# Kernel optimization log

Hardware: AMD Instinct MI355X
Metric: run time of the kernel (lower is better)

Reference implementation:

```python
import jax, jax.numpy as jnp
import numpy as np

NUM_USERS = 100000
NUM_ITEMS = 100000
D = 64
B, P, N, NB, NN = 1024, 32, 64, 32, 32
W1, W2, W3 = 1.0, 0.1, 1.0


def setup_inputs() -> dict:
    key = jax.random.key(0)
    ks = jax.random.split(key, 12)
    u2e = 0.1 + 0.03 * jax.random.normal(ks[0], (NUM_USERS, D), jnp.float32)
    v2e = 0.1 + 0.03 * jax.random.normal(ks[1], (NUM_ITEMS, D), jnp.float32)
    margin_uv = jnp.ones((NUM_USERS, 1), jnp.float32)
    margin_vv = jnp.ones((NUM_ITEMS, 1), jnp.float32)
    margin_uu = jnp.ones((NUM_USERS, 1), jnp.float32)
    train_u = jax.random.randint(ks[2], (B,), 0, NUM_USERS)
    pos_idx = jax.random.randint(ks[3], (B, P), 0, NUM_ITEMS)
    neg_idx = jax.random.randint(ks[4], (B, N), 0, NUM_ITEMS)
    nb_idx = jax.random.randint(ks[5], (B, NB), 0, NUM_USERS)
    nn_idx = jax.random.randint(ks[6], (B, NN), 0, NUM_USERS)
    # ragged lengths -> padded masks
    def mk_mask(k, maxlen):
        lens = jax.random.randint(k, (B,), 1, maxlen + 1)
        return jnp.arange(maxlen)[None, :] < lens[:, None]
    pos_mask = mk_mask(ks[7], P)
    neg_mask = mk_mask(ks[8], N)
    nb_mask = mk_mask(ks[9], NB)
    nn_mask = mk_mask(ks[10], NN)
    return dict(u2e=u2e, v2e=v2e, margin_uv=margin_uv, margin_vv=margin_vv,
                margin_uu=margin_uu, train_u=train_u, pos_idx=pos_idx,
                neg_idx=neg_idx, nb_idx=nb_idx, nn_idx=nn_idx,
                pos_mask=pos_mask, neg_mask=neg_mask, nb_mask=nb_mask,
                nn_mask=nn_mask)


def reference(u2e, v2e, margin_uv, margin_vv, margin_uu, train_u, pos_idx,
              neg_idx, nb_idx, nn_idx, pos_mask, neg_mask, nb_mask, nn_mask):
    u_e = u2e[train_u]            # [B,D]
    p_e = v2e[pos_idx]            # [B,P,D]
    n_e = v2e[neg_idx]            # [B,N,D]
    nb_e = u2e[nb_idx]            # [B,NB,D]
    nn_e = u2e[nn_idx]            # [B,NN,D]
    pm = pos_mask.astype(u_e.dtype)
    nm = neg_mask.astype(u_e.dtype)
    nbm = nb_mask.astype(u_e.dtype)
    nnm = nn_mask.astype(u_e.dtype)

    # user-item triplet loss: hinge[b,i,k] = m_u[b] + ||u-p_i||^2 - ||u-n_k||^2
    d1 = jnp.sum((u_e[:, None, :] - p_e) ** 2, -1)   # [B,P]
    d2 = jnp.sum((u_e[:, None, :] - n_e) ** 2, -1)   # [B,N]
    m_u = margin_uv[train_u, 0]                       # [B]
    uv = jax.nn.relu(m_u[:, None, None] + d1[:, :, None] - d2[:, None, :])
    uv_loss = jnp.sum(uv * (pm[:, :, None] * nm[:, None, :]))

    # item-item loss (torch broadcast: margin over a separate positive axis j)
    # hinge[b,i,j,k] = m_v[b,j] + ||p_i-u||^2 - ||p_i-n_k||^2
    p2 = jnp.sum(p_e ** 2, -1)                        # [B,P]
    n2 = jnp.sum(n_e ** 2, -1)                        # [B,N]
    d2v = p2[:, :, None] + n2[:, None, :] - 2.0 * jnp.einsum('bpd,bnd->bpn', p_e, n_e)
    m_v = margin_vv[pos_idx, 0]                       # [B,P]
    hinge_vv = jax.nn.relu(m_v[:, None, :, None] + d1[:, :, None, None] - d2v[:, :, None, :])
    mask_vv = pm[:, :, None, None] * pm[:, None, :, None] * nm[:, None, None, :]
    vv_loss = jnp.sum(hinge_vv * mask_vv)

    # user-user social loss
    d1s = jnp.sum((u_e[:, None, :] - nb_e) ** 2, -1)  # [B,NB]
    d2s = jnp.sum((u_e[:, None, :] - nn_e) ** 2, -1)  # [B,NN]
    m_s = margin_uu[train_u, 0]                       # [B]
    uu = jax.nn.relu(m_s[:, None, None] + d1s[:, :, None] - d2s[:, None, :])
    uu_loss = jnp.sum(uu * (nbm[:, :, None] * nnm[:, None, :]))

    # margin regularizer (masked mean over batch positives)
    loss_am = (jnp.mean(margin_uv[train_u])
               + jnp.sum(m_v * pm) / jnp.sum(pm)
               + jnp.mean(margin_uu[train_u]))

    return uv_loss + W1 * vv_loss + W3 * uu_loss + W2 * loss_am
```

## Files before the change

kernel.cpp:

```cpp
#include <hip/hip_runtime.h>
#include <cfloat>

#define BB   1024
#define PP   32
#define NNEG 64
#define DD   64
#define BSTR 72
#define SSTR 66

static constexpr float W2c = 0.1f;

typedef __attribute__((ext_vector_type(8)))  short bf16x8;
typedef __attribute__((ext_vector_type(16))) float f32x16;

__device__ __forceinline__ short f2bf(float f) {
    unsigned u = __float_as_uint(f);
    unsigned r = (u + 0x7fffu + ((u >> 16) & 1u)) >> 16;
    return (short)r;
}

__device__ __forceinline__ float parse_mask(const void* p, int flag, int j) {
    if (flag == 1) return ((const unsigned char*)p)[j] ? 1.0f : 0.0f;
    if (flag == 2) return (((const float*)p)[j] != 0.0f) ? 1.0f : 0.0f;
    return ((const int*)p)[j] ? 1.0f : 0.0f;
}

__global__ __launch_bounds__(512, 8) void loss_kernel(
    const float* __restrict__ u2e, const float* __restrict__ v2e,
    const float* __restrict__ margin_uv, const float* __restrict__ margin_vv,
    const float* __restrict__ margin_uu,
    const int* __restrict__ train_u, const int* __restrict__ pos_idx,
    const int* __restrict__ neg_idx, const int* __restrict__ nb_idx,
    const int* __restrict__ nn_idx,
    const void* __restrict__ pos_mask, const void* __restrict__ neg_mask,
    const void* __restrict__ nb_mask, const void* __restrict__ nn_mask,
    float* __restrict__ ws) {

    const int b = blockIdx.x;
    const int t = threadIdx.x;
    const int lane = t & 63;
    const int w = t >> 6;

    __shared__ __align__(16) short pn_bf[96 * BSTR];
    __shared__ __align__(16) float s_lds[PP * SSTR];
    __shared__ float d1[PP], p2s[PP], d2[NNEG], n2s[NNEG], d1sA[PP], d2sA[PP];
    __shared__ float pmf[PP], nmf[NNEG], nbmf[PP], nnmf[PP];
    __shared__ float mvp[PP], mv_arr[PP], s_srt[PP], S_suf[PP + 1];
    __shared__ float sc[2];
    __shared__ float red[8][3];

    int flag = 0;
    if (w < 3) {
        unsigned f32h = 0, byth = 0;
        #pragma unroll
        for (int i2 = 0; i2 < 16; ++i2) {
            unsigned mw = ((const unsigned int*)pos_mask)[lane + 64 * i2];
            f32h |= (mw == 0x3f800000u) ? 1u : 0u;
            byth |= ((mw != 0x3f800000u) && (mw & 0xFFFFFF00u)) ? 1u : 0u;
        }
        flag = __any(f32h) ? 2 : (__any(byth) ? 1 : 0);
    }

    const int tu  = train_u[b];
    const int q   = t & 15;
    const int R0  = t >> 4;
    const int gi0 = pos_idx[b * PP + R0];
    const int gi1 = neg_idx[b * NNEG + R0];
    const int gi2 = neg_idx[b * NNEG + R0 + 32];
    const int row = t >> 3, sub = t & 7;
    const int sidx = (row < PP) ? nb_idx[b * PP + row] : nn_idx[b * PP + row - PP];

    const float* uR = u2e + (size_t)tu * DD;
    const float4 u4 = *(const float4*)(uR + 4 * q);
    float4 ch0 = *(const float4*)(v2e + (size_t)gi0 * DD + 4 * q);
    float4 ch1 = *(const float4*)(v2e + (size_t)gi1 * DD + 4 * q);
    float4 ch2 = *(const float4*)(v2e + (size_t)gi2 * DD + 4 * q);
    const float* rp = u2e + (size_t)sidx * DD + 8 * sub;
    const float4 e0 = *(const float4*)(rp);
    const float4 e1 = *(const float4*)(rp + 4);
    const float4 v0 = *(const float4*)(uR + 8 * sub);
    const float4 v1 = *(const float4*)(uR + 8 * sub + 4);

    {
        float sdp[3], sqp[3];
        float dx, dy, dz, dw;
        dx = ch0.x-u4.x; dy = ch0.y-u4.y; dz = ch0.z-u4.z; dw = ch0.w-u4.w;
        sdp[0] = dx*dx+dy*dy+dz*dz+dw*dw;
        sqp[0] = ch0.x*ch0.x+ch0.y*ch0.y+ch0.z*ch0.z+ch0.w*ch0.w;
        dx = ch1.x-u4.x; dy = ch1.y-u4.y; dz = ch1.z-u4.z; dw = ch1.w-u4.w;
        sdp[1] = dx*dx+dy*dy+dz*dz+dw*dw;
        sqp[1] = ch1.x*ch1.x+ch1.y*ch1.y+ch1.z*ch1.z+ch1.w*ch1.w;
        dx = ch2.x-u4.x; dy = ch2.y-u4.y; dz = ch2.z-u4.z; dw = ch2.w-u4.w;
        sdp[2] = dx*dx+dy*dy+dz*dz+dw*dw;
        sqp[2] = ch2.x*ch2.x+ch2.y*ch2.y+ch2.z*ch2.z+ch2.w*ch2.w;
        #pragma unroll
        for (int m = 1; m < 16; m <<= 1) {
            #pragma unroll
            for (int r = 0; r < 3; ++r) {
                sdp[r] += __shfl_xor(sdp[r], m);
                sqp[r] += __shfl_xor(sqp[r], m);
            }
        }
        if (q == 0) {
            d1[R0]      = sdp[0]; p2s[R0]      = sqp[0];
            d2[R0]      = sdp[1]; n2s[R0]      = sqp[1];
            d2[R0 + 32] = sdp[2]; n2s[R0 + 32] = sqp[2];
        }
    }
    {
        float dx = e0.x-v0.x, dy = e0.y-v0.y, dz = e0.z-v0.z, dw = e0.w-v0.w;
        float s = dx*dx+dy*dy+dz*dz+dw*dw;
        dx = e1.x-v1.x; dy = e1.y-v1.y; dz = e1.z-v1.z; dw = e1.w-v1.w;
        s += dx*dx+dy*dy+dz*dz+dw*dw;
        s += __shfl_xor(s, 1);
        s += __shfl_xor(s, 2);
        s += __shfl_xor(s, 4);
        if (sub == 0) { if (row < PP) d1sA[row] = s; else d2sA[row - PP] = s; }
    }
    if (t < PP) {
        float pm = parse_mask(pos_mask, flag, b * PP + t);
        float mv = margin_vv[pos_idx[b * PP + t]];
        pmf[t] = pm; mv_arr[t] = mv;
        mvp[t] = (pm != 0.0f) ? mv : -FLT_MAX;
    } else if (t < 96) {
        nmf[t - PP] = parse_mask(neg_mask, flag, b * NNEG + (t - PP));
    } else if (t < 128) {
        nbmf[t - 96] = parse_mask(nb_mask, flag, b * PP + (t - 96));
    } else if (t < 160) {
        nnmf[t - 128] = parse_mask(nn_mask, flag, b * PP + (t - 128));
    }
    if (t == 0) { sc[0] = margin_uv[tu]; sc[1] = margin_uu[tu]; }
    {
        short4 s0 = make_short4(f2bf(ch0.x), f2bf(ch0.y), f2bf(ch0.z), f2bf(ch0.w));
        short4 s1 = make_short4(f2bf(ch1.x), f2bf(ch1.y), f2bf(ch1.z), f2bf(ch1.w));
        short4 s2 = make_short4(f2bf(ch2.x), f2bf(ch2.y), f2bf(ch2.z), f2bf(ch2.w));
        *(short4*)(pn_bf + R0 * BSTR + 4 * q)        = s0;
        *(short4*)(pn_bf + (R0 + 32) * BSTR + 4 * q) = s1;
        *(short4*)(pn_bf + (R0 + 64) * BSTR + 4 * q) = s2;
    }
    __syncthreads();

    if (w < 2) {
        f32x16 acc;
        #pragma unroll
        for (int i = 0; i < 16; ++i) acc[i] = 0.0f;
        const int lr = lane & 31;
        const int hi = lane >> 5;
        const short* ap = pn_bf + lr * BSTR;
        const short* bp = pn_bf + (PP + 32 * w + lr) * BSTR;
        #pragma unroll
        for (int c = 0; c < 4; ++c) {
            const int d0 = 16 * c + 8 * hi;
            bf16x8 a   = *(const bf16x8*)(ap + d0);
            bf16x8 bfr = *(const bf16x8*)(bp + d0);
            acc = __builtin_amdgcn_mfma_f32_32x32x16_bf16(a, bfr, acc, 0, 0, 0);
        }
        #pragma unroll
        for (int r = 0; r < 16; ++r) {
            const int m = (r & 3) + 8 * (r >> 2) + 4 * hi;
            s_lds[m * SSTR + 32 * w + lr] = acc[r];
        }
    } else if (w == 2 && lane < PP) {
        float vj = mvp[lane];
        int r = 0;
        #pragma unroll
        for (int j = 0; j < PP; ++j) {
            float o = mvp[j];
            r += (o < vj || (o == vj && j < lane)) ? 1 : 0;
        }
        s_srt[r] = vj;
        __threadfence_block();
        float y = s_srt[lane];
        #pragma unroll
        for (int d = 1; d < PP; d <<= 1) {
            float z = __shfl_down(y, d);
            if (lane + d < PP) y += z;
        }
        S_suf[lane] = y;
        if (lane == 0) S_suf[PP] = 0.0f;
    }
    __syncthreads();

    const float m_u = sc[0], m_s = sc[1];
    const float s31 = s_srt[PP - 1];
    const int kb = t & 15;
    const int i  = R0;
    const float d1i = d1[i], p2i = p2s[i], pmi = pmf[i];
    float loss = 0.0f;
    #pragma unroll
    for (int c = 0; c < 4; ++c) {
        const int k = kb + 16 * c;
        const float Sik = s_lds[i * SSTR + k];
        const float cc = d1i - (p2i + n2s[k] - 2.0f * Sik);
        const float v = -cc;
        int t0 = 0;
        #pragma unroll
        for (int st = 16; st > 0; st >>= 1)
            t0 += (s_srt[t0 + st - 1] <= v) ? st : 0;
        t0 += (s31 <= v) ? 1 : 0;
        const float inner = S_suf[t0] + (float)(PP - t0) * cc;
        const float uvh = fmaxf(m_u + d1i - d2[k], 0.0f);
        loss += pmi * nmf[k] * (inner + uvh);
    }

    #pragma unroll
    for (int rr = 0; rr < 2; ++rr) {
        int pid = t + 512 * rr;
        int ii = pid >> 5, k = pid & 31;
        loss += nbmf[ii] * nnmf[k] * fmaxf(m_s + d1sA[ii] - d2sA[k], 0.0f);
    }

    float a2 = (t < PP) ? mv_arr[t] * pmf[t] : 0.0f;
    float a3 = (t < PP) ? pmf[t] : 0.0f;
    #pragma unroll
    for (int m = 1; m < 64; m <<= 1) {
        loss += __shfl_xor(loss, m);
        a2   += __shfl_xor(a2, m);
        a3   += __shfl_xor(a3, m);
    }
    if (lane == 0) { red[w][0] = loss; red[w][1] = a2; red[w][2] = a3; }
    __syncthreads();
    if (t == 0) {
        float S0 = 0, S2 = 0, S3 = 0;
        #pragma unroll
        for (int i2 = 0; i2 < 8; ++i2) { S0 += red[i2][0]; S2 += red[i2][1]; S3 += red[i2][2]; }
        ws[0 * BB + b] = S0;
        ws[1 * BB + b] = sc[0];
        ws[2 * BB + b] = S2;
        ws[3 * BB + b] = S3;
        ws[4 * BB + b] = sc[1];
    }
}

__global__ __launch_bounds__(64) void finalize_kernel(const float* __restrict__ ws,
                                                      float* __restrict__ out) {
    const int lane = threadIdx.x;
    float s[5];
    #pragma unroll
    for (int a = 0; a < 5; ++a) {
        const float4* w4 = (const float4*)(ws + a * BB);
        float acc = 0.0f;
        #pragma unroll
        for (int j = 0; j < 4; ++j) {
            float4 v = w4[lane + 64 * j];
            acc += v.x + v.y + v.z + v.w;
        }
        s[a] = acc;
    }
    #pragma unroll
    for (int m = 1; m < 64; m <<= 1)
        #pragma unroll
        for (int a = 0; a < 5; ++a) s[a] += __shfl_xor(s[a], m);
    if (lane == 0) {
        float loss_am = s[1] / (float)BB + s[2] / s[3] + s[4] / (float)BB;
        out[0] = s[0] + W2c * loss_am;
    }
}

extern "C" void kernel_launch(void* const* d_in, const int* in_sizes, int n_in,
                              void* d_out, int out_size, void* d_ws, size_t ws_size,
                              hipStream_t stream) {
    const float* u2e       = (const float*)d_in[0];
    const float* v2e       = (const float*)d_in[1];
    const float* margin_uv = (const float*)d_in[2];
    const float* margin_vv = (const float*)d_in[3];
    const float* margin_uu = (const float*)d_in[4];
    const int*   train_u   = (const int*)d_in[5];
    const int*   pos_idx   = (const int*)d_in[6];
    const int*   neg_idx   = (const int*)d_in[7];
    const int*   nb_idx    = (const int*)d_in[8];
    const int*   nn_idx    = (const int*)d_in[9];
    const void*  pos_mask  = d_in[10];
    const void*  neg_mask  = d_in[11];
    const void*  nb_mask   = d_in[12];
    const void*  nn_mask   = d_in[13];

    float* ws  = (float*)d_ws;
    float* out = (float*)d_out;

    loss_kernel<<<BB, 512, 0, stream>>>(u2e, v2e, margin_uv, margin_vv, margin_uu,
                                        train_u, pos_idx, neg_idx, nb_idx, nn_idx,
                                        pos_mask, neg_mask, nb_mask, nn_mask, ws);
    finalize_kernel<<<1, 64, 0, stream>>>(ws, out);
}
```

Baseline: 19.84 us.

## Consume MFMA accumulators in registers and drop the final block barrier

The loss kernel now evaluates the hinge/rank-search loss directly on the MFMA accumulator registers instead of spilling the P×N dot products to LDS. This removes the s_lds buffer, one __syncthreads, and the block-wide reduction. Work is split by wave: waves 0-1 handle item losses, waves 2-3 the social loss, and wave 4 the margin sums, with each wave writing partials straight to the workspace. The margin sort and suffix-scan move into wave 0 ahead of the MFMA barrier, the mask-type probe reads fewer words, and finalize uses 256 threads to reduce the larger partial array. The cost is idle waves 5-7 and a heavier serial tail on waves 0-1.

Result: slower. 21.04 us (+6.0%).

```diff
diff --git a/kernel.cpp b/kernel.cpp
--- a/kernel.cpp
+++ b/kernel.cpp
@@ -6,7 +6,11 @@
 #define NNEG 64
 #define DD   64
 #define BSTR 72
-#define SSTR 66
+
+#define WS_MU 4096
+#define WS_A2 5120
+#define WS_A3 6144
+#define WS_MS 7168
 
 static constexpr float W2c = 0.1f;
 
@@ -42,18 +46,15 @@
     const int w = t >> 6;
 
     __shared__ __align__(16) short pn_bf[96 * BSTR];
-    __shared__ __align__(16) float s_lds[PP * SSTR];
     __shared__ float d1[PP], p2s[PP], d2[NNEG], n2s[NNEG], d1sA[PP], d2sA[PP];
     __shared__ float pmf[PP], nmf[NNEG], nbmf[PP], nnmf[PP];
     __shared__ float mvp[PP], mv_arr[PP], s_srt[PP], S_suf[PP + 1];
-    __shared__ float sc[2];
-    __shared__ float red[8][3];
 
     int flag = 0;
     if (w < 3) {
         unsigned f32h = 0, byth = 0;
         #pragma unroll
-        for (int i2 = 0; i2 < 16; ++i2) {
+        for (int i2 = 0; i2 < 4; ++i2) {
             unsigned mw = ((const unsigned int*)pos_mask)[lane + 64 * i2];
             f32h |= (mw == 0x3f800000u) ? 1u : 0u;
             byth |= ((mw != 0x3f800000u) && (mw & 0xFFFFFF00u)) ? 1u : 0u;
@@ -117,19 +118,45 @@
         s += __shfl_xor(s, 4);
         if (sub == 0) { if (row < PP) d1sA[row] = s; else d2sA[row - PP] = s; }
     }
-    if (t < PP) {
-        float pm = parse_mask(pos_mask, flag, b * PP + t);
-        float mv = margin_vv[pos_idx[b * PP + t]];
-        pmf[t] = pm; mv_arr[t] = mv;
-        mvp[t] = (pm != 0.0f) ? mv : -FLT_MAX;
-    } else if (t < 96) {
-        nmf[t - PP] = parse_mask(neg_mask, flag, b * NNEG + (t - PP));
-    } else if (t < 128) {
-        nbmf[t - 96] = parse_mask(nb_mask, flag, b * PP + (t - 96));
-    } else if (t < 160) {
-        nnmf[t - 128] = parse_mask(nn_mask, flag, b * PP + (t - 128));
-    }
-    if (t == 0) { sc[0] = margin_uv[tu]; sc[1] = margin_uu[tu]; }
+    if (w == 0) {
+        if (lane < PP) {
+            float pm = parse_mask(pos_mask, flag, b * PP + lane);
+            float mv = margin_vv[pos_idx[b * PP + lane]];
+            pmf[lane] = pm; mv_arr[lane] = mv;
+            mvp[lane] = (pm != 0.0f) ? mv : -FLT_MAX;
+        } else {
+            nmf[lane - PP] = parse_mask(neg_mask, flag, b * NNEG + (lane - PP));
+        }
+    } else if (w == 1) {
+        if (lane < PP) nmf[PP + lane] = parse_mask(neg_mask, flag, b * NNEG + PP + lane);
+        else           nbmf[lane - PP] = parse_mask(nb_mask, flag, b * PP + (lane - PP));
+    } else if (w == 2 && lane < PP) {
+        nnmf[lane] = parse_mask(nn_mask, flag, b * PP + lane);
+    }
+    if (w == 0) {
+        __threadfence_block();
+        if (lane < PP) {
+            float vj = mvp[lane];
+            int r = 0;
+            #pragma unroll
+            for (int j = 0; j < PP; ++j) {
+                float o = mvp[j];
+                r += (o < vj || (o == vj && j < lane)) ? 1 : 0;
+            }
+            s_srt[r] = vj;
+        }
+        __threadfence_block();
+        if (lane < PP) {
+            float y = s_srt[lane];
+            #pragma unroll
+            for (int d = 1; d < PP; d <<= 1) {
+                float z = __shfl_down(y, d);
+                if (lane + d < PP) y += z;
+            }
+            S_suf[lane] = y;
+            if (lane == 0) S_suf[PP] = 0.0f;
+        }
+    }
     {
         short4 s0 = make_short4(f2bf(ch0.x), f2bf(ch0.y), f2bf(ch0.z), f2bf(ch0.w));
         short4 s1 = make_short4(f2bf(ch1.x), f2bf(ch1.y), f2bf(ch1.z), f2bf(ch1.w));
@@ -155,105 +182,92 @@
             bf16x8 bfr = *(const bf16x8*)(bp + d0);
             acc = __builtin_amdgcn_mfma_f32_32x32x16_bf16(a, bfr, acc, 0, 0, 0);
         }
+        const float m_u = margin_uv[tu];
+        const int   k   = 32 * w + lr;
+        const float d2k = d2[k], n2k = n2s[k], nmk = nmf[k];
+        const float s31 = s_srt[PP - 1];
+        float loss = 0.0f;
         #pragma unroll
         for (int r = 0; r < 16; ++r) {
-            const int m = (r & 3) + 8 * (r >> 2) + 4 * hi;
-            s_lds[m * SSTR + 32 * w + lr] = acc[r];
-        }
-    } else if (w == 2 && lane < PP) {
-        float vj = mvp[lane];
-        int r = 0;
-        #pragma unroll
-        for (int j = 0; j < PP; ++j) {
-            float o = mvp[j];
-            r += (o < vj || (o == vj && j < lane)) ? 1 : 0;
-        }
-        s_srt[r] = vj;
-        __threadfence_block();
-        float y = s_srt[lane];
-        #pragma unroll
-        for (int d = 1; d < PP; d <<= 1) {
-            float z = __shfl_down(y, d);
-            if (lane + d < PP) y += z;
-        }
-        S_suf[lane] = y;
-        if (lane == 0) S_suf[PP] = 0.0f;
-    }
-    __syncthreads();
-
-    const float m_u = sc[0], m_s = sc[1];
-    const float s31 = s_srt[PP - 1];
-    const int kb = t & 15;
-    const int i  = R0;
-    const float d1i = d1[i], p2i = p2s[i], pmi = pmf[i];
-    float loss = 0.0f;
+            const int i = (r & 3) + 8 * (r >> 2) + 4 * hi;
+            const float cc = d1[i] - (p2s[i] + n2k - 2.0f * acc[r]);
+            const float v = -cc;
+            int t0 = 0;
+            #pragma unroll
+            for (int st = 16; st > 0; st >>= 1)
+                t0 += (s_srt[t0 + st - 1] <= v) ? st : 0;
+            t0 += (s31 <= v) ? 1 : 0;
+            const float inner = S_suf[t0] + (float)(PP - t0) * cc;
+            const float uvh = fmaxf(m_u + d1[i] - d2k, 0.0f);
+            loss += pmf[i] * nmk * (inner + uvh);
+        }
+        #pragma unroll
+        for (int m = 1; m < 64; m <<= 1) loss += __shfl_xor(loss, m);
+        if (lane == 0) ws[b * 4 + w] = loss;
+        if (w == 0 && lane == 0) {
+            ws[WS_MU + b] = m_u;
+            ws[WS_MS + b] = margin_uu[tu];
+        }
+    } else if (w < 4) {
+        const float m_s = margin_uu[tu];
+        const int base = (w - 2) * 512;
+        float loss = 0.0f;
+        #pragma unroll
+        for (int j2 = 0; j2 < 8; ++j2) {
+            const int pid = base + lane + 64 * j2;
+            const int ii = pid >> 5, k = pid & 31;
+            loss += nbmf[ii] * nnmf[k] * fmaxf(m_s + d1sA[ii] - d2sA[k], 0.0f);
+        }
+        #pragma unroll
+        for (int m = 1; m < 64; m <<= 1) loss += __shfl_xor(loss, m);
+        if (lane == 0) ws[b * 4 + w] = loss;
+    } else if (w == 4) {
+        float a2 = (lane < PP) ? mv_arr[lane] * pmf[lane] : 0.0f;
+        float a3 = (lane < PP) ? pmf[lane] : 0.0f;
+        #pragma unroll
+        for (int m = 1; m < 64; m <<= 1) {
+            a2 += __shfl_xor(a2, m);
+            a3 += __shfl_xor(a3, m);
+        }
+        if (lane == 0) { ws[WS_A2 + b] = a2; ws[WS_A3 + b] = a3; }
+    }
+}
+
+__global__ __launch_bounds__(256) void finalize_kernel(const float* __restrict__ ws,
+                                                       float* __restrict__ out) {
+    __shared__ float red[4][5];
+    const int t = threadIdx.x, lane = t & 63, w = t >> 6;
+    float s0 = 0, s1 = 0, s2 = 0, s3 = 0, s4 = 0;
     #pragma unroll
-    for (int c = 0; c < 4; ++c) {
-        const int k = kb + 16 * c;
-        const float Sik = s_lds[i * SSTR + k];
-        const float cc = d1i - (p2i + n2s[k] - 2.0f * Sik);
-        const float v = -cc;
-        int t0 = 0;
-        #pragma unroll
-        for (int st = 16; st > 0; st >>= 1)
-            t0 += (s_srt[t0 + st - 1] <= v) ? st : 0;
-        t0 += (s31 <= v) ? 1 : 0;
-        const float inner = S_suf[t0] + (float)(PP - t0) * cc;
-        const float uvh = fmaxf(m_u + d1i - d2[k], 0.0f);
-        loss += pmi * nmf[k] * (inner + uvh);
-    }
-
+    for (int j = 0; j < 16; ++j) s0 += ws[t + 256 * j];
     #pragma unroll
-    for (int rr = 0; rr < 2; ++rr) {
-        int pid = t + 512 * rr;
-        int ii = pid >> 5, k = pid & 31;
-        loss += nbmf[ii] * nnmf[k] * fmaxf(m_s + d1sA[ii] - d2sA[k], 0.0f);
-    }
-
-    float a2 = (t < PP) ? mv_arr[t] * pmf[t] : 0.0f;
-    float a3 = (t < PP) ? pmf[t] : 0.0f;
+    for (int j = 0; j < 4; ++j) {
+        const int i = t + 256 * j;
+        s1 += ws[WS_MU + i];
+        s2 += ws[WS_A2 + i];
+        s3 += ws[WS_A3 + i];
+        s4 += ws[WS_MS + i];
+    }
     #pragma unroll
     for (int m = 1; m < 64; m <<= 1) {
-        loss += __shfl_xor(loss, m);
-        a2   += __shfl_xor(a2, m);
-        a3   += __shfl_xor(a3, m);
-    }
-    if (lane == 0) { red[w][0] = loss; red[w][1] = a2; red[w][2] = a3; }
+        s0 += __shfl_xor(s0, m); s1 += __shfl_xor(s1, m);
+        s2 += __shfl_xor(s2, m); s3 += __shfl_xor(s3, m);
+        s4 += __shfl_xor(s4, m);
+    }
+    if (lane == 0) {
+        red[w][0] = s0; red[w][1] = s1; red[w][2] = s2;
+        red[w][3] = s3; red[w][4] = s4;
+    }
     __syncthreads();
     if (t == 0) {
-        float S0 = 0, S2 = 0, S3 = 0;
-        #pragma unroll
-        for (int i2 = 0; i2 < 8; ++i2) { S0 += red[i2][0]; S2 += red[i2][1]; S3 += red[i2][2]; }
-        ws[0 * BB + b] = S0;
-        ws[1 * BB + b] = sc[0];
-        ws[2 * BB + b] = S2;
-        ws[3 * BB + b] = S3;
-        ws[4 * BB + b] = sc[1];
-    }
-}
-
-__global__ __launch_bounds__(64) void finalize_kernel(const float* __restrict__ ws,
-                                                      float* __restrict__ out) {
-    const int lane = threadIdx.x;
-    float s[5];
-    #pragma unroll
-    for (int a = 0; a < 5; ++a) {
-        const float4* w4 = (const float4*)(ws + a * BB);
-        float acc = 0.0f;
-        #pragma unroll
-        for (int j = 0; j < 4; ++j) {
-            float4 v = w4[lane + 64 * j];
-            acc += v.x + v.y + v.z + v.w;
-        }
-        s[a] = acc;
-    }
-    #pragma unroll
-    for (int m = 1; m < 64; m <<= 1)
-        #pragma unroll
-        for (int a = 0; a < 5; ++a) s[a] += __shfl_xor(s[a], m);
-    if (lane == 0) {
-        float loss_am = s[1] / (float)BB + s[2] / s[3] + s[4] / (float)BB;
-        out[0] = s[0] + W2c * loss_am;
+        float S[5];
+        #pragma unroll
+        for (int a = 0; a < 5; ++a) {
+            S[a] = 0;
+            for (int i = 0; i < 4; ++i) S[a] += red[i][a];
+        }
+        float loss_am = S[1] / (float)BB + S[2] / S[3] + S[4] / (float)BB;
+        out[0] = S[0] + W2c * loss_am;
     }
 }
 
@@ -281,5 +295,5 @@
     loss_kernel<<<BB, 512, 0, stream>>>(u2e, v2e, margin_uv, margin_vv, margin_uu,
                                         train_u, pos_idx, neg_idx, nb_idx, nn_idx,
                                         pos_mask, neg_mask, nb_mask, nn_mask, ws);
-    finalize_kernel<<<1, 64, 0, stream>>>(ws, out);
-}
+    finalize_kernel<<<1, 256, 0, stream>>>(ws, out);
+}
```
